# Performance work log

Hardware: AMD Instinct MI355X
Metric: run time of the kernel (lower is better)

The kernel has to match this reference:

```python
import jax, jax.numpy as jnp
import numpy as np
from jax import lax

GAMMA = 1.0  # init kwarg

def setup_inputs() -> dict:
    key = jax.random.key(0)
    k1, k2 = jax.random.split(key)
    B, L, D = 64, 256, 1024
    return {
        "student_tokens": jax.random.normal(k1, (B, L, D), jnp.float32),
        "teacher_tokens": jax.random.normal(k2, (B, L, D), jnp.float32),
    }

def _soft_dtw(dist, gamma):
    # dist: (B, LS, LT). Returns R[:, LS, LT] of the soft-DTW DP.
    B, LS, LT = dist.shape
    inf = jnp.array(jnp.inf, dist.dtype)

    def cell(r_left, inputs):
        d, r_diag, r_up = inputs  # each (B,)
        stacked = jnp.stack([r_diag, r_up, r_left], axis=-1)  # (B, 3)
        softmin = -gamma * jax.nn.logsumexp(-stacked / gamma, axis=-1)
        r = d + softmin
        return r, r

    def row_step(prev_row, dist_row):
        # prev_row: (B, LT+1) = R[i-1, :]; dist_row: (B, LT) = dist[:, i-1, :]
        xs = (dist_row.T, prev_row[:, :-1].T, prev_row[:, 1:].T)  # each (LT, B)
        r0 = jnp.full((B,), inf, dist.dtype)  # R[i, 0] = inf
        _, row = lax.scan(cell, r0, xs)  # (LT, B)
        new_row = jnp.concatenate([r0[:, None], row.T], axis=1)  # (B, LT+1)
        return new_row, None

    init_row = jnp.concatenate(
        [jnp.zeros((B, 1), dist.dtype), jnp.full((B, LT), inf, dist.dtype)], axis=1
    )  # R[0, :] = [0, inf, ..., inf]
    final_row, _ = lax.scan(row_step, init_row, jnp.swapaxes(dist, 0, 1))
    return final_row[:, -1]  # R[:, LS, LT]

def reference(student_tokens, teacher_tokens):
    # torch.cdist(p=2) via the expanded quadratic form (avoids (B,L,L,D) blowup)
    s2 = jnp.sum(student_tokens * student_tokens, axis=-1)  # (B, LS)
    t2 = jnp.sum(teacher_tokens * teacher_tokens, axis=-1)  # (B, LT)
    sq = (s2[:, :, None] + t2[:, None, :]
          - 2.0 * jnp.einsum('bld,bmd->blm', student_tokens, teacher_tokens))
    dist = jnp.sqrt(jnp.maximum(sq, 1e-12))  # (B, LS, LT)
    return _soft_dtw(dist, GAMMA).mean()
```

## Files before the change

kernel.cpp:

```cpp
#include <hip/hip_runtime.h>
#include <math.h>

#define BB 64
#define LL 256
#define DD 1024
#define NDPAD 512
#define BK 32
#define LOG2E 1.4426950408889634f
#define LN2   0.6931471805599453f

typedef __attribute__((ext_vector_type(8))) short short8v;
typedef __attribute__((ext_vector_type(4))) float float4v;

__device__ __forceinline__ unsigned short f2bf(float f) {
    unsigned u = __float_as_uint(f);
    unsigned r = (u + 0x7fffu + ((u >> 16) & 1u)) >> 16;
    return (unsigned short)r;
}
__device__ __forceinline__ float bf2f(unsigned short u) {
    return __uint_as_float(((unsigned)u) << 16);
}
__device__ __forceinline__ unsigned cvtpk(float lo, float hi) {
    unsigned r;
    asm("v_cvt_pk_bf16_f32 %0, %1, %2" : "=v"(r) : "v"(lo), "v"(hi));
    return r;
}

__global__ __launch_bounds__(512) void fused_kernel(const float* __restrict__ S,
                                                    const float* __restrict__ T,
                                                    unsigned short* __restrict__ Dd) {
    __shared__ unsigned short lds[2][2][2][128 * BK];
    __shared__ float nrmP[2][2][128];

    const int b    = blockIdx.x;
    const int tile = blockIdx.y;
    const int i0 = (tile & 1) * 128;
    const int j0 = (tile >> 1) * 128;
    const int tid = threadIdx.x, w = tid >> 6, lane = tid & 63;
    const int p = w >> 2;
    const int q = w & 3;
    const int wr = q >> 1, wc = q & 1;
    const int kbase = p * 512;

    const float* Sg = S + ((size_t)b * LL + i0) * DD;
    const float* Tg = T + ((size_t)b * LL + j0) * DD;

    const int sr   = q * 16 + (lane >> 2);
    const int slot = lane & 3;
    const int kb   = slot ^ ((sr >> 1) & 3);

    float4v acc[4][4];
    const float4v fzero = {0.f, 0.f, 0.f, 0.f};
    #pragma unroll
    for (int mi = 0; mi < 4; ++mi)
        #pragma unroll
        for (int ni = 0; ni < 4; ++ni) acc[mi][ni] = fzero;

    struct Stg { float4 a[2][2]; float4 bb[2][2]; };
    Stg st0, st1;
    float ns[2][2] = {};

    auto issue = [&](Stg& s, int kt) {
        const float* pa = Sg + (size_t)sr * DD + kbase + kt * BK + kb * 8;
        const float* pb = Tg + (size_t)sr * DD + kbase + kt * BK + kb * 8;
        s.a[0][0]  = *(const float4*)(pa);
        s.a[0][1]  = *(const float4*)(pa + 4);
        s.a[1][0]  = *(const float4*)(pa + 64 * DD);
        s.a[1][1]  = *(const float4*)(pa + 64 * DD + 4);
        s.bb[0][0] = *(const float4*)(pb);
        s.bb[0][1] = *(const float4*)(pb + 4);
        s.bb[1][0] = *(const float4*)(pb + 64 * DD);
        s.bb[1][1] = *(const float4*)(pb + 64 * DD + 4);
    };

    auto cvtwrite = [&](const float4& v0, const float4& v1, unsigned short* dst, float& nacc) {
        nacc += v0.x * v0.x + v0.y * v0.y + v0.z * v0.z + v0.w * v0.w
              + v1.x * v1.x + v1.y * v1.y + v1.z * v1.z + v1.w * v1.w;
        uint4 o;
        o.x = cvtpk(v0.x, v0.y);
        o.y = cvtpk(v0.z, v0.w);
        o.z = cvtpk(v1.x, v1.y);
        o.w = cvtpk(v1.z, v1.w);
        *(uint4*)dst = o;
    };

    auto commit = [&](Stg& s, int buf) {
        #pragma unroll
        for (int n = 0; n < 2; ++n) {
            cvtwrite(s.a[n][0],  s.a[n][1],  &lds[p][buf][0][(n * 64 + sr) * BK + slot * 8], ns[0][n]);
            cvtwrite(s.bb[n][0], s.bb[n][1], &lds[p][buf][1][(n * 64 + sr) * BK + slot * 8], ns[1][n]);
        }
    };

    auto compute = [&](int buf) {
        const unsigned short* LA = &lds[p][buf][0][0];
        const unsigned short* LB = &lds[p][buf][1][0];
        short8v af[4], bf[4];
        #pragma unroll
        for (int mi = 0; mi < 4; ++mi) {
            int row = wr * 64 + mi * 16 + (lane & 15);
            int kbf = (lane >> 4) ^ ((row >> 1) & 3);
            af[mi] = *(const short8v*)(LA + row * BK + kbf * 8);
        }
        #pragma unroll
        for (int ni = 0; ni < 4; ++ni) {
            int row = wc * 64 + ni * 16 + (lane & 15);
            int kbf = (lane >> 4) ^ ((row >> 1) & 3);
            bf[ni] = *(const short8v*)(LB + row * BK + kbf * 8);
        }
        #pragma unroll
        for (int mi = 0; mi < 4; ++mi)
            #pragma unroll
            for (int ni = 0; ni < 4; ++ni)
                acc[mi][ni] = __builtin_amdgcn_mfma_f32_16x16x32_bf16(af[mi], bf[ni],
                                                                      acc[mi][ni], 0, 0, 0);
    };

    auto phase_barrier = [&]() {
        asm volatile("s_waitcnt lgkmcnt(0)" ::: "memory");
        __builtin_amdgcn_s_barrier();
        __builtin_amdgcn_sched_barrier(0);
    };

    issue(st0, 0);
    for (int kt2 = 0; kt2 < 16; kt2 += 2) {
        issue(st1, kt2 + 1);
        commit(st0, 0);
        phase_barrier();
        compute(0);
        if (kt2 + 2 < 16) issue(st0, kt2 + 2);
        commit(st1, 1);
        phase_barrier();
        compute(1);
    }

    #pragma unroll
    for (int side = 0; side < 2; ++side)
        #pragma unroll
        for (int n = 0; n < 2; ++n) {
            float s = ns[side][n];
            s += __shfl_xor(s, 1, 64);
            s += __shfl_xor(s, 2, 64);
            if (slot == 0) nrmP[p][side][n * 64 + sr] = s;
        }
    __syncthreads();

    float* cb = (float*)&lds[0][0][0][0];
    if (p == 1) {
        #pragma unroll
        for (int mi = 0; mi < 4; ++mi)
            #pragma unroll
            for (int ni = 0; ni < 4; ++ni)
                *(float4v*)(cb + q * 4096 + (mi * 4 + ni) * 256 + lane * 4) = acc[mi][ni];
    }
    __syncthreads();

    if (p == 0) {
        #pragma unroll
        for (int mi = 0; mi < 4; ++mi)
            #pragma unroll
            for (int ni = 0; ni < 4; ++ni)
                acc[mi][ni] += *(const float4v*)(cb + q * 4096 + (mi * 4 + ni) * 256 + lane * 4);

        const int r0 = (lane >> 4) * 4;
        const int cf = lane & 15;
        unsigned short* Db = Dd + (size_t)b * NDPAD * 256;
        #pragma unroll
        for (int mi = 0; mi < 4; ++mi) {
            #pragma unroll
            for (int ni = 0; ni < 4; ++ni) {
                int lj = wc * 64 + ni * 16 + cf;
                float tj = nrmP[0][1][lj] + nrmP[1][1][lj];
                int j = j0 + lj;
                #pragma unroll
                for (int rg = 0; rg < 4; ++rg) {
                    int li = wr * 64 + mi * 16 + r0 + rg;
                    float sq = nrmP[0][0][li] + nrmP[1][0][li] + tj - 2.0f * acc[mi][ni][rg];
                    float dv = sqrtf(fmaxf(sq, 1e-12f));
                    int i = i0 + li;
                    Db[(size_t)(i + j) * 256 + j] = f2bf(dv * LOG2E);
                }
            }
        }
    }
}


__device__ __forceinline__ float wshr1(float src, float fill) {
    return __int_as_float(__builtin_amdgcn_update_dpp(
        __float_as_int(fill), __float_as_int(src), 0x138, 0xF, 0xF, false));
}

__global__ __launch_bounds__(256) void sdtw_kernel(const unsigned short* __restrict__ Dg,
                                                   float* __restrict__ res) {
    __shared__ unsigned short sd[8][16 * 256];
    __shared__ float bbuf[3][2][16];
    const int b = blockIdx.x;
    const int tid = threadIdx.x;
    const int w = tid >> 6;
    const int lane = tid & 63;
    const float INF = INFINITY;
    const unsigned short* Db = Dg + (size_t)b * NDPAD * 256;

    auto prefetch = [&](int c) {
        #pragma unroll
        for (int q = 0; q < 8; ++q) {
            __builtin_amdgcn_global_load_lds(
                (const __attribute__((address_space(1))) void*)(Db + (size_t)c * 4096 + q * 512 + lane * 8),
                (__attribute__((address_space(3))) void*)(&sd[c & 7][q * 512]),
                16, 0, 0);
        }
    };

    const int col0 = 64 * w + lane;
    float rm1 = INF, rm2 = INF;
    float p2carry = (tid == 0) ? 0.0f : INF;
    float bcarry = INF;

    if (w == 0) {
        prefetch(0);
        prefetch(1);
        asm volatile("s_waitcnt vmcnt(8)" ::: "memory");
    }
    asm volatile("s_waitcnt lgkmcnt(0)" ::: "memory");
    __builtin_amdgcn_s_barrier();

    for (int r = 0; r < 35; ++r) {
        if (w == 0 && r + 2 < 32) prefetch(r + 2);
        const int c = r - w;
        if (0 <= c && c < 32) {
            const unsigned short* Lp = &sd[c & 7][0];
            float dv[16];
            #pragma unroll
            for (int q = 0; q < 16; ++q)
                dv[q] = bf2f(Lp[q * 256 + col0]);

            float bv[16];
            if (w == 0) {
                #pragma unroll
                for (int q = 0; q < 16; ++q) bv[q] = INF;
            } else {
                const float4* bp4 = (const float4*)&bbuf[w - 1][c & 1][0];
                float4 b0 = bp4[0], b1 = bp4[1], b2 = bp4[2], b3 = bp4[3];
                bv[0] = bcarry;
                bv[1] = b0.x;  bv[2] = b0.y;  bv[3] = b0.z;  bv[4] = b0.w;
                bv[5] = b1.x;  bv[6] = b1.y;  bv[7] = b1.z;  bv[8] = b1.w;
                bv[9] = b2.x;  bv[10] = b2.y; bv[11] = b2.z; bv[12] = b2.w;
                bv[13] = b3.x; bv[14] = b3.y; bv[15] = b3.z;
                bcarry = b3.w;
            }
            asm volatile("s_waitcnt lgkmcnt(0)" ::: "memory");
            __builtin_amdgcn_sched_barrier(0);

            const int ibase = 16 * c - col0;
            float bb[16];
            #pragma unroll
            for (int q = 0; q < 16; ++q) {
                float p1 = wshr1(rm1, bv[q]);
                float p2 = p2carry;
                p2carry = p1;
                float m   = fminf(p2, fminf(rm1, p1));
                float mid = __builtin_amdgcn_fmed3f(p2, rm1, p1);
                float M   = fmaxf(p2, fmaxf(rm1, p1));
                float s   = (__builtin_amdgcn_exp2f(m - mid) +
                             __builtin_amdgcn_exp2f(m - M)) + 1.0f;
                float rcv = dv[q] + m - __builtin_amdgcn_logf(s);
                bool valid = (unsigned)(ibase + q) < 256u;
                rcv = valid ? rcv : INF;
                rm2 = rm1;
                rm1 = rcv;
                bb[q] = rcv;
            }
            if (w < 3 && lane == 63) {
                float4* op = (float4*)&bbuf[w][c & 1][0];
                op[0] = make_float4(bb[0], bb[1], bb[2], bb[3]);
                op[1] = make_float4(bb[4], bb[5], bb[6], bb[7]);
                op[2] = make_float4(bb[8], bb[9], bb[10], bb[11]);
                op[3] = make_float4(bb[12], bb[13], bb[14], bb[15]);
            }
        }
        if (w == 0) {
            if (r < 30) asm volatile("s_waitcnt vmcnt(8)" ::: "memory");
            else        asm volatile("s_waitcnt vmcnt(0)" ::: "memory");
        }
        asm volatile("s_waitcnt lgkmcnt(0)" ::: "memory");
        __builtin_amdgcn_s_barrier();
    }
    if (tid == 255) res[b] = rm2 * LN2;
}

__global__ void reduce_kernel(const float* __restrict__ res, float* __restrict__ out) {
    int t = threadIdx.x;
    float v = res[t];
    #pragma unroll
    for (int off = 32; off; off >>= 1) v += __shfl_down(v, off, 64);
    if (t == 0) out[0] = v * (1.0f / BB);
}

extern "C" void kernel_launch(void* const* d_in, const int* in_sizes, int n_in,
                              void* d_out, int out_size, void* d_ws, size_t ws_size,
                              hipStream_t stream) {
    const float* S = (const float*)d_in[0];
    const float* T = (const float*)d_in[1];

    const size_t nDiag = (size_t)BB * NDPAD * 256;
    unsigned short* diag = (unsigned short*)d_ws;
    float* rsv = (float*)(diag + nDiag);

    fused_kernel<<<dim3(BB, 4), 512, 0, stream>>>(S, T, diag);
    sdtw_kernel<<<BB, 256, 0, stream>>>(diag, rsv);
    reduce_kernel<<<1, 64, 0, stream>>>(rsv, (float*)d_out);
}
```

Measured before the change: 75.28 us.

## Warp-specialize GEMM into producer loader waves and consumer MFMA waves

Replaces the split-K scheme, where two groups of four waves each covered half of K and then reduced through LDS, with producer/consumer specialization. Waves 0-3 load fp32 tiles from global memory, convert them to bf16, accumulate the norms and write LDS. Waves 4-7 run the MFMAs over the full K range and do the epilogue. This removes the cross-group accumulator reduction and halves the LDS footprint, but only half the waves issue MFMAs, and each K step is serialized through two block-wide barriers.

Result: slower. 78.06 us (+3.7%).

```diff
diff --git a/kernel.cpp b/kernel.cpp
--- a/kernel.cpp
+++ b/kernel.cpp
@@ -29,25 +29,24 @@
 __global__ __launch_bounds__(512) void fused_kernel(const float* __restrict__ S,
                                                     const float* __restrict__ T,
                                                     unsigned short* __restrict__ Dd) {
-    __shared__ unsigned short lds[2][2][2][128 * BK];
-    __shared__ float nrmP[2][2][128];
+    __shared__ unsigned short lds[2][2][128 * BK];
+    __shared__ float nrm[2][128];
 
     const int b    = blockIdx.x;
     const int tile = blockIdx.y;
     const int i0 = (tile & 1) * 128;
     const int j0 = (tile >> 1) * 128;
     const int tid = threadIdx.x, w = tid >> 6, lane = tid & 63;
-    const int p = w >> 2;
-    const int q = w & 3;
-    const int wr = q >> 1, wc = q & 1;
-    const int kbase = p * 512;
 
     const float* Sg = S + ((size_t)b * LL + i0) * DD;
     const float* Tg = T + ((size_t)b * LL + j0) * DD;
 
+    const int q  = w & 3;
     const int sr   = q * 16 + (lane >> 2);
     const int slot = lane & 3;
     const int kb   = slot ^ ((sr >> 1) & 3);
+
+    const int wr = q >> 1, wc = q & 1;
 
     float4v acc[4][4];
     const float4v fzero = {0.f, 0.f, 0.f, 0.f};
@@ -61,8 +60,8 @@
     float ns[2][2] = {};
 
     auto issue = [&](Stg& s, int kt) {
-        const float* pa = Sg + (size_t)sr * DD + kbase + kt * BK + kb * 8;
-        const float* pb = Tg + (size_t)sr * DD + kbase + kt * BK + kb * 8;
+        const float* pa = Sg + (size_t)sr * DD + kt * BK + kb * 8;
+        const float* pb = Tg + (size_t)sr * DD + kt * BK + kb * 8;
         s.a[0][0]  = *(const float4*)(pa);
         s.a[0][1]  = *(const float4*)(pa + 4);
         s.a[1][0]  = *(const float4*)(pa + 64 * DD);
@@ -87,14 +86,14 @@
     auto commit = [&](Stg& s, int buf) {
         #pragma unroll
         for (int n = 0; n < 2; ++n) {
-            cvtwrite(s.a[n][0],  s.a[n][1],  &lds[p][buf][0][(n * 64 + sr) * BK + slot * 8], ns[0][n]);
-            cvtwrite(s.bb[n][0], s.bb[n][1], &lds[p][buf][1][(n * 64 + sr) * BK + slot * 8], ns[1][n]);
+            cvtwrite(s.a[n][0],  s.a[n][1],  &lds[buf][0][(n * 64 + sr) * BK + slot * 8], ns[0][n]);
+            cvtwrite(s.bb[n][0], s.bb[n][1], &lds[buf][1][(n * 64 + sr) * BK + slot * 8], ns[1][n]);
         }
     };
 
     auto compute = [&](int buf) {
-        const unsigned short* LA = &lds[p][buf][0][0];
-        const unsigned short* LB = &lds[p][buf][1][0];
+        const unsigned short* LA = &lds[buf][0][0];
+        const unsigned short* LB = &lds[buf][1][0];
         short8v af[4], bf[4];
         #pragma unroll
         for (int mi = 0; mi < 4; ++mi) {
@@ -116,52 +115,50 @@
                                                                       acc[mi][ni], 0, 0, 0);
     };
 
-    auto phase_barrier = [&]() {
+    auto pbar = [&]() {
         asm volatile("s_waitcnt lgkmcnt(0)" ::: "memory");
         __builtin_amdgcn_s_barrier();
         __builtin_amdgcn_sched_barrier(0);
     };
 
-    issue(st0, 0);
-    for (int kt2 = 0; kt2 < 16; kt2 += 2) {
-        issue(st1, kt2 + 1);
+    if (w < 4) {
+        issue(st0, 0);
+        issue(st1, 1);
         commit(st0, 0);
-        phase_barrier();
-        compute(0);
-        if (kt2 + 2 < 16) issue(st0, kt2 + 2);
-        commit(st1, 1);
-        phase_barrier();
-        compute(1);
-    }
-
-    #pragma unroll
-    for (int side = 0; side < 2; ++side)
-        #pragma unroll
-        for (int n = 0; n < 2; ++n) {
-            float s = ns[side][n];
-            s += __shfl_xor(s, 1, 64);
-            s += __shfl_xor(s, 2, 64);
-            if (slot == 0) nrmP[p][side][n * 64 + sr] = s;
-        }
+    }
+    pbar();
+
+    for (int kt = 0; kt < 32; kt += 2) {
+        if (w < 4) {
+            if (kt + 2 < 32) issue(st0, kt + 2);
+            commit(st1, 1);
+        } else {
+            compute(0);
+        }
+        pbar();
+        if (w < 4) {
+            if (kt + 3 < 32) issue(st1, kt + 3);
+            if (kt + 2 < 32) commit(st0, 0);
+        } else {
+            compute(1);
+        }
+        pbar();
+    }
+
+    if (w < 4) {
+        #pragma unroll
+        for (int side = 0; side < 2; ++side)
+            #pragma unroll
+            for (int n = 0; n < 2; ++n) {
+                float s = ns[side][n];
+                s += __shfl_xor(s, 1, 64);
+                s += __shfl_xor(s, 2, 64);
+                if (slot == 0) nrm[side][n * 64 + sr] = s;
+            }
+    }
     __syncthreads();
 
-    float* cb = (float*)&lds[0][0][0][0];
-    if (p == 1) {
-        #pragma unroll
-        for (int mi = 0; mi < 4; ++mi)
-            #pragma unroll
-            for (int ni = 0; ni < 4; ++ni)
-                *(float4v*)(cb + q * 4096 + (mi * 4 + ni) * 256 + lane * 4) = acc[mi][ni];
-    }
-    __syncthreads();
-
-    if (p == 0) {
-        #pragma unroll
-        for (int mi = 0; mi < 4; ++mi)
-            #pragma unroll
-            for (int ni = 0; ni < 4; ++ni)
-                acc[mi][ni] += *(const float4v*)(cb + q * 4096 + (mi * 4 + ni) * 256 + lane * 4);
-
+    if (w >= 4) {
         const int r0 = (lane >> 4) * 4;
         const int cf = lane & 15;
         unsigned short* Db = Dd + (size_t)b * NDPAD * 256;
@@ -170,12 +167,12 @@
             #pragma unroll
             for (int ni = 0; ni < 4; ++ni) {
                 int lj = wc * 64 + ni * 16 + cf;
-                float tj = nrmP[0][1][lj] + nrmP[1][1][lj];
+                float tj = nrm[1][lj];
                 int j = j0 + lj;
                 #pragma unroll
                 for (int rg = 0; rg < 4; ++rg) {
                     int li = wr * 64 + mi * 16 + r0 + rg;
-                    float sq = nrmP[0][0][li] + nrmP[1][0][li] + tj - 2.0f * acc[mi][ni][rg];
+                    float sq = nrm[0][li] + tj - 2.0f * acc[mi][ni][rg];
                     float dv = sqrtf(fmaxf(sq, 1e-12f));
                     int i = i0 + li;
                     Db[(size_t)(i + j) * 256 + j] = f2bf(dv * LOG2E);
@@ -184,7 +181,6 @@
         }
     }
 }
-
 
 __device__ __forceinline__ float wshr1(float src, float fill) {
     return __int_as_float(__builtin_amdgcn_update_dpp(
```

## Fuse distance GEMM and soft-DTW into one kernel with per-tile flags

Applied to the files above, without the earlier changes.

The distance-tile kernel and the soft-DTW kernel are merged into a single 256-block launch. Each block signals completion of its tile through a global atomic flag, and the tile-0 block of each batch then runs the DP wavefront. It waits on the other tiles' flags only when its prefetch first reaches their anti-diagonals. This removes a kernel launch boundary and lets the DP start before all distance tiles are written. The cost is spin-waiting, an extra memset, and reliance on all four tile blocks of a batch being co-resident or scheduled first. The DP now runs with 512 threads, of which waves 4-7 idle, and the prefetch vmcnt thresholds are deepened.

New measurement: 132.9 us. 76.6% more time.

```diff
diff --git a/kernel.cpp b/kernel.cpp
--- a/kernel.cpp
+++ b/kernel.cpp
@@ -25,15 +25,25 @@
     asm("v_cvt_pk_bf16_f32 %0, %1, %2" : "=v"(r) : "v"(lo), "v"(hi));
     return r;
 }
-
-__global__ __launch_bounds__(512) void fused_kernel(const float* __restrict__ S,
-                                                    const float* __restrict__ T,
-                                                    unsigned short* __restrict__ Dd) {
-    __shared__ unsigned short lds[2][2][2][128 * BK];
-    __shared__ float nrmP[2][2][128];
-
-    const int b    = blockIdx.x;
-    const int tile = blockIdx.y;
+__device__ __forceinline__ float wshr1(float src, float fill) {
+    return __int_as_float(__builtin_amdgcn_update_dpp(
+        __float_as_int(fill), __float_as_int(src), 0x138, 0xF, 0xF, false));
+}
+
+__global__ __launch_bounds__(512) void mega_kernel(const float* __restrict__ S,
+                                                   const float* __restrict__ T,
+                                                   unsigned short* __restrict__ Dd,
+                                                   int* __restrict__ flags,
+                                                   float* __restrict__ res) {
+    __shared__ __align__(16) unsigned char smem[67968];
+    auto LDSU = [&](int p, int buf, int ab) -> unsigned short* {
+        return (unsigned short*)smem + ((p * 4 + buf * 2 + ab) * 128 * BK);
+    };
+    float* nrmB = (float*)(smem + 65536);
+
+    const int bid  = blockIdx.x;
+    const int b    = bid & 63;
+    const int tile = bid >> 6;
     const int i0 = (tile & 1) * 128;
     const int j0 = (tile >> 1) * 128;
     const int tid = threadIdx.x, w = tid >> 6, lane = tid & 63;
@@ -87,14 +97,14 @@
     auto commit = [&](Stg& s, int buf) {
         #pragma unroll
         for (int n = 0; n < 2; ++n) {
-            cvtwrite(s.a[n][0],  s.a[n][1],  &lds[p][buf][0][(n * 64 + sr) * BK + slot * 8], ns[0][n]);
-            cvtwrite(s.bb[n][0], s.bb[n][1], &lds[p][buf][1][(n * 64 + sr) * BK + slot * 8], ns[1][n]);
+            cvtwrite(s.a[n][0],  s.a[n][1],  LDSU(p, buf, 0) + (n * 64 + sr) * BK + slot * 8, ns[0][n]);
+            cvtwrite(s.bb[n][0], s.bb[n][1], LDSU(p, buf, 1) + (n * 64 + sr) * BK + slot * 8, ns[1][n]);
         }
     };
 
     auto compute = [&](int buf) {
-        const unsigned short* LA = &lds[p][buf][0][0];
-        const unsigned short* LB = &lds[p][buf][1][0];
+        const unsigned short* LA = LDSU(p, buf, 0);
+        const unsigned short* LB = LDSU(p, buf, 1);
         short8v af[4], bf[4];
         #pragma unroll
         for (int mi = 0; mi < 4; ++mi) {
@@ -141,11 +151,11 @@
             float s = ns[side][n];
             s += __shfl_xor(s, 1, 64);
             s += __shfl_xor(s, 2, 64);
-            if (slot == 0) nrmP[p][side][n * 64 + sr] = s;
+            if (slot == 0) nrmB[(p * 2 + side) * 128 + n * 64 + sr] = s;
         }
     __syncthreads();
 
-    float* cb = (float*)&lds[0][0][0][0];
+    float* cb = (float*)smem;
     if (p == 1) {
         #pragma unroll
         for (int mi = 0; mi < 4; ++mi)
@@ -170,12 +180,12 @@
             #pragma unroll
             for (int ni = 0; ni < 4; ++ni) {
                 int lj = wc * 64 + ni * 16 + cf;
-                float tj = nrmP[0][1][lj] + nrmP[1][1][lj];
+                float tj = nrmB[1 * 128 + lj] + nrmB[3 * 128 + lj];
                 int j = j0 + lj;
                 #pragma unroll
                 for (int rg = 0; rg < 4; ++rg) {
                     int li = wr * 64 + mi * 16 + r0 + rg;
-                    float sq = nrmP[0][0][li] + nrmP[1][0][li] + tj - 2.0f * acc[mi][ni][rg];
+                    float sq = nrmB[0 * 128 + li] + nrmB[2 * 128 + li] + tj - 2.0f * acc[mi][ni][rg];
                     float dv = sqrtf(fmaxf(sq, 1e-12f));
                     int i = i0 + li;
                     Db[(size_t)(i + j) * 256 + j] = f2bf(dv * LOG2E);
@@ -183,36 +193,37 @@
             }
         }
     }
-}
-
-
-__device__ __forceinline__ float wshr1(float src, float fill) {
-    return __int_as_float(__builtin_amdgcn_update_dpp(
-        __float_as_int(fill), __float_as_int(src), 0x138, 0xF, 0xF, false));
-}
-
-__global__ __launch_bounds__(256) void sdtw_kernel(const unsigned short* __restrict__ Dg,
-                                                   float* __restrict__ res) {
-    __shared__ unsigned short sd[8][16 * 256];
-    __shared__ float bbuf[3][2][16];
-    const int b = blockIdx.x;
-    const int tid = threadIdx.x;
-    const int w = tid >> 6;
-    const int lane = tid & 63;
+
+    __threadfence();
+    __syncthreads();
+    if (tid == 0) atomicAdd(&flags[4 * b + tile], 1);
+
+    if (tile != 0) return;
+
+    __syncthreads();
+    unsigned short* sdb = (unsigned short*)smem;
+    float* bbuf = (float*)(smem + 65536);
+    const unsigned short* Db = Dd + (size_t)b * NDPAD * 256;
     const float INF = INFINITY;
-    const unsigned short* Db = Dg + (size_t)b * NDPAD * 256;
 
     auto prefetch = [&](int c) {
         #pragma unroll
-        for (int q = 0; q < 8; ++q) {
+        for (int qq = 0; qq < 8; ++qq) {
             __builtin_amdgcn_global_load_lds(
-                (const __attribute__((address_space(1))) void*)(Db + (size_t)c * 4096 + q * 512 + lane * 8),
-                (__attribute__((address_space(3))) void*)(&sd[c & 7][q * 512]),
+                (const __attribute__((address_space(1))) void*)(Db + (size_t)c * 4096 + qq * 512 + lane * 8),
+                (__attribute__((address_space(3))) void*)(sdb + (c & 7) * 4096 + qq * 512),
                 16, 0, 0);
         }
     };
-
-    const int col0 = 64 * w + lane;
+    auto waitflag = [&](int idx) {
+        if (lane == 0) {
+            while (atomicAdd(&flags[idx], 0) == 0) __builtin_amdgcn_s_sleep(16);
+        }
+        __threadfence();
+    };
+
+    const int cw   = (w < 4) ? w : 64;
+    const int col0 = 64 * (w & 3) + lane;
     float rm1 = INF, rm2 = INF;
     float p2carry = (tid == 0) ? 0.0f : INF;
     float bcarry = INF;
@@ -226,21 +237,25 @@
     __builtin_amdgcn_s_barrier();
 
     for (int r = 0; r < 35; ++r) {
-        if (w == 0 && r + 2 < 32) prefetch(r + 2);
-        const int c = r - w;
+        if (w == 0 && r + 2 < 32) {
+            if (r + 2 == 8)  { waitflag(4 * b + 1); waitflag(4 * b + 2); }
+            if (r + 2 == 16) { waitflag(4 * b + 3); }
+            prefetch(r + 2);
+        }
+        const int c = r - cw;
         if (0 <= c && c < 32) {
-            const unsigned short* Lp = &sd[c & 7][0];
+            const unsigned short* Lp = sdb + (c & 7) * 4096;
             float dv[16];
             #pragma unroll
-            for (int q = 0; q < 16; ++q)
-                dv[q] = bf2f(Lp[q * 256 + col0]);
+            for (int qq = 0; qq < 16; ++qq)
+                dv[qq] = bf2f(Lp[qq * 256 + col0]);
 
             float bv[16];
             if (w == 0) {
                 #pragma unroll
-                for (int q = 0; q < 16; ++q) bv[q] = INF;
+                for (int qq = 0; qq < 16; ++qq) bv[qq] = INF;
             } else {
-                const float4* bp4 = (const float4*)&bbuf[w - 1][c & 1][0];
+                const float4* bp4 = (const float4*)(bbuf + ((w - 1) * 2 + (c & 1)) * 16);
                 float4 b0 = bp4[0], b1 = bp4[1], b2 = bp4[2], b3 = bp4[3];
                 bv[0] = bcarry;
                 bv[1] = b0.x;  bv[2] = b0.y;  bv[3] = b0.z;  bv[4] = b0.w;
@@ -255,8 +270,8 @@
             const int ibase = 16 * c - col0;
             float bb[16];
             #pragma unroll
-            for (int q = 0; q < 16; ++q) {
-                float p1 = wshr1(rm1, bv[q]);
+            for (int qq = 0; qq < 16; ++qq) {
+                float p1 = wshr1(rm1, bv[qq]);
                 float p2 = p2carry;
                 p2carry = p1;
                 float m   = fminf(p2, fminf(rm1, p1));
@@ -264,15 +279,15 @@
                 float M   = fmaxf(p2, fmaxf(rm1, p1));
                 float s   = (__builtin_amdgcn_exp2f(m - mid) +
                              __builtin_amdgcn_exp2f(m - M)) + 1.0f;
-                float rcv = dv[q] + m - __builtin_amdgcn_logf(s);
-                bool valid = (unsigned)(ibase + q) < 256u;
+                float rcv = dv[qq] + m - __builtin_amdgcn_logf(s);
+                bool valid = (unsigned)(ibase + qq) < 256u;
                 rcv = valid ? rcv : INF;
                 rm2 = rm1;
                 rm1 = rcv;
-                bb[q] = rcv;
+                bb[qq] = rcv;
             }
             if (w < 3 && lane == 63) {
-                float4* op = (float4*)&bbuf[w][c & 1][0];
+                float4* op = (float4*)(bbuf + (w * 2 + (c & 1)) * 16);
                 op[0] = make_float4(bb[0], bb[1], bb[2], bb[3]);
                 op[1] = make_float4(bb[4], bb[5], bb[6], bb[7]);
                 op[2] = make_float4(bb[8], bb[9], bb[10], bb[11]);
@@ -280,8 +295,9 @@
             }
         }
         if (w == 0) {
-            if (r < 30) asm volatile("s_waitcnt vmcnt(8)" ::: "memory");
-            else        asm volatile("s_waitcnt vmcnt(0)" ::: "memory");
+            if (r < 30)       asm volatile("s_waitcnt vmcnt(16)" ::: "memory");
+            else if (r == 30) asm volatile("s_waitcnt vmcnt(8)" ::: "memory");
+            else if (r == 31) asm volatile("s_waitcnt vmcnt(0)" ::: "memory");
         }
         asm volatile("s_waitcnt lgkmcnt(0)" ::: "memory");
         __builtin_amdgcn_s_barrier();
@@ -305,9 +321,10 @@
 
     const size_t nDiag = (size_t)BB * NDPAD * 256;
     unsigned short* diag = (unsigned short*)d_ws;
-    float* rsv = (float*)(diag + nDiag);
-
-    fused_kernel<<<dim3(BB, 4), 512, 0, stream>>>(S, T, diag);
-    sdtw_kernel<<<BB, 256, 0, stream>>>(diag, rsv);
+    float* rsv  = (float*)(diag + nDiag);
+    int*   flags = (int*)(rsv + 64);
+
+    hipMemsetAsync(flags, 0, 256 * sizeof(int), stream);
+    mega_kernel<<<4 * BB, 512, 0, stream>>>(S, T, diag, flags, rsv);
     reduce_kernel<<<1, 64, 0, stream>>>(rsv, (float*)d_out);
 }
```
